# Optimization experiments

Measured on AMD Instinct MI355X. Metric: run time of the kernel, lower is better.

The kernel has to match this reference:

```python
import jax, jax.numpy as jnp
import numpy as np

VOCAB = 267735
CUTOFFS = [0, 20000, 40000, 200000, 267735]
D_EMBED = 1024
D_PROJ = 1024
DIV_VAL = 4
EMB_SCALE = float(D_PROJ) ** 0.5


def setup_inputs() -> dict:
    key = jax.random.key(0)
    ks = jax.random.split(key, 9)
    input_ids = jax.random.randint(ks[0], (8, 2048), 0, VOCAB, dtype=jnp.int64)
    inp = {"input_ids": input_ids}
    for i in range(4):
        l, r = CUTOFFS[i], CUTOFFS[i + 1]
        d_i = D_EMBED // (DIV_VAL ** i)
        inp[f"emb{i}"] = jax.random.normal(ks[1 + 2 * i], (r - l, d_i), dtype=jnp.float32) * 0.02
        inp[f"proj{i}"] = jax.random.normal(ks[2 + 2 * i], (D_PROJ, d_i), dtype=jnp.float32) * 0.02
    return inp


def reference(input_ids, emb0, emb1, emb2, emb3, proj0, proj1, proj2, proj3):
    tables = [emb0, emb1, emb2, emb3]
    projs = [proj0, proj1, proj2, proj3]
    out = jnp.zeros(input_ids.shape + (D_PROJ,), dtype=jnp.float32)
    for i in range(4):
        l, r = CUTOFFS[i], CUTOFFS[i + 1]
        mask = (input_ids >= l) & (input_ids < r)                     # [B,S]
        idx = jnp.clip(input_ids - l, 0, r - l - 1)                   # [B,S]
        emb_i = tables[i][idx]                                        # [B,S,d_i]
        proj_i = jnp.einsum('bse,de->bsd', emb_i, projs[i])           # [B,S,D]
        out = out + jnp.where(mask[..., None], proj_i, 0.0)
    return out * EMB_SCALE
```

## Files before the change

### kernel.cpp

```cpp
#include <hip/hip_runtime.h>


constexpr int NTOK  = 16384;
constexpr int DPROJ = 1024;
constexpr float EMB_SCALE = 32.0f;

typedef __attribute__((ext_vector_type(8))) short short8;
typedef __attribute__((ext_vector_type(4))) float float4v;

__global__ __launch_bounds__(256) void partition_kernel(
    const int* __restrict__ ids, int* __restrict__ cnt, int* __restrict__ lists)
{
    int t = blockIdx.x * 256 + threadIdx.x;
    int id = ids[t];
    int c = (id >= 200000) ? 3 : (id >= 40000) ? 2 : (id >= 20000) ? 1 : 0;
    int lane = threadIdx.x & 63;
    unsigned long long lt = (1ull << lane) - 1ull;
    int pos = 0;
#pragma unroll
    for (int i = 0; i < 4; ++i) {
        unsigned long long m = __ballot(c == i);
        int b = 0;
        if (lane == 0 && m) b = atomicAdd(&cnt[i], (int)__popcll(m));
        b = __shfl(b, 0);
        if (c == i) pos = b + (int)__popcll(m & lt);
    }
    lists[c * NTOK + pos] = t;
}

__device__ __forceinline__ short f2bf(float f) {
    unsigned u = __builtin_bit_cast(unsigned, f);
    u += 0x7FFFu + ((u >> 16) & 1u);
    return (short)(u >> 16);
}

template<int D>
__device__ __forceinline__ void gemm_tile(
    const int* __restrict__ ids,
    const float* __restrict__ emb,
    const float* __restrict__ proj,
    const int* __restrict__ list,
    int count, int lo,
    float* __restrict__ out,
    short (*Asm)[40], short (*Bsm)[40], int* smTok, int* smRow)
{
    const int m0 = blockIdx.y * 64;
    if (m0 >= count) return;
    const int n0 = blockIdx.x * 128;
    const int tid  = threadIdx.x;
    const int lane = tid & 63;
    const int wv   = tid >> 6;
    const int col  = lane & 15;
    const int quad = lane >> 4;

    if (tid < 64) {
        int m = m0 + tid;
        int tok = (m < count) ? list[m] : -1;
        smTok[tid] = tok;
        smRow[tid] = (tok >= 0) ? (ids[tok] - lo) : 0;
    }
    __syncthreads();

    const int ar = tid >> 2, ac = (tid & 3) * 8;
    const int br = tid >> 1, bc = (tid & 1) * 16;
    const float* arow = emb  + (size_t)smRow[ar] * D + ac;
    const float* brow = proj + (size_t)(n0 + br) * D + bc;

    float4v acc[4][2] = {};

    constexpr int CHUNKS = (D + 31) / 32;
    for (int kc = 0; kc < CHUNKS; ++kc) {
        const int k0 = kc * 32;
        float4 a0 = {}, a1 = {}, b0 = {}, b1 = {}, b2 = {}, b3 = {};
        if (ac + 0  < D || D >= 32) {  }
        if (D >= 32 || ac + 0  < D) a0 = *(const float4*)(arow + k0);
        if (D >= 32 || ac + 4  < D) a1 = *(const float4*)(arow + k0 + 4);
        if (D >= 32 || bc + 0  < D) b0 = *(const float4*)(brow + k0);
        if (D >= 32 || bc + 4  < D) b1 = *(const float4*)(brow + k0 + 4);
        if (D >= 32 || bc + 8  < D) b2 = *(const float4*)(brow + k0 + 8);
        if (D >= 32 || bc + 12 < D) b3 = *(const float4*)(brow + k0 + 12);
        if (D == 16) {
            if (ac >= 16) { a0 = float4{}; a1 = float4{}; }
            if (bc >= 16) { b0 = float4{}; b1 = float4{}; b2 = float4{}; b3 = float4{}; }
        }
        __syncthreads();
        {
            short8 va = { f2bf(a0.x), f2bf(a0.y), f2bf(a0.z), f2bf(a0.w),
                          f2bf(a1.x), f2bf(a1.y), f2bf(a1.z), f2bf(a1.w) };
            *(short8*)&Asm[ar][ac] = va;
            short8 vb0 = { f2bf(b0.x), f2bf(b0.y), f2bf(b0.z), f2bf(b0.w),
                           f2bf(b1.x), f2bf(b1.y), f2bf(b1.z), f2bf(b1.w) };
            short8 vb1 = { f2bf(b2.x), f2bf(b2.y), f2bf(b2.z), f2bf(b2.w),
                           f2bf(b3.x), f2bf(b3.y), f2bf(b3.z), f2bf(b3.w) };
            *(short8*)&Bsm[br][bc]     = vb0;
            *(short8*)&Bsm[br][bc + 8] = vb1;
        }
        __syncthreads();

        short8 af[4], bf[2];
#pragma unroll
        for (int m = 0; m < 4; ++m)
            af[m] = *(const short8*)&Asm[m * 16 + col][quad * 8];
#pragma unroll
        for (int n = 0; n < 2; ++n)
            bf[n] = *(const short8*)&Bsm[wv * 32 + n * 16 + col][quad * 8];
#pragma unroll
        for (int m = 0; m < 4; ++m)
#pragma unroll
            for (int n = 0; n < 2; ++n)
                acc[m][n] = __builtin_amdgcn_mfma_f32_16x16x32_bf16(
                    af[m], bf[n], acc[m][n], 0, 0, 0);
    }

#pragma unroll
    for (int m = 0; m < 4; ++m) {
#pragma unroll
        for (int r = 0; r < 4; ++r) {
            int tok = smTok[m * 16 + quad * 4 + r];
            if (tok < 0) continue;
            float* op = out + (size_t)tok * DPROJ + n0 + wv * 32 + col;
            op[0]  = acc[m][0][r] * EMB_SCALE;
            op[16] = acc[m][1][r] * EMB_SCALE;
        }
    }
}

__global__ __launch_bounds__(256) void adaptive_emb_gemm(
    const int* __restrict__ ids,
    const float* __restrict__ e0, const float* __restrict__ p0,
    const float* __restrict__ e1, const float* __restrict__ p1,
    const float* __restrict__ e2, const float* __restrict__ p2,
    const float* __restrict__ e3, const float* __restrict__ p3,
    const int* __restrict__ cnt, const int* __restrict__ lists,
    float* __restrict__ out)
{
    __shared__ short Asm[64][40];
    __shared__ short Bsm[128][40];
    __shared__ int smTok[64];
    __shared__ int smRow[64];

    switch (blockIdx.z) {
    case 0: gemm_tile<1024>(ids, e0, p0, lists,          cnt[0], 0,      out, Asm, Bsm, smTok, smRow); break;
    case 1: gemm_tile<256> (ids, e1, p1, lists + NTOK,   cnt[1], 20000,  out, Asm, Bsm, smTok, smRow); break;
    case 2: gemm_tile<64>  (ids, e2, p2, lists + 2*NTOK, cnt[2], 40000,  out, Asm, Bsm, smTok, smRow); break;
    case 3: gemm_tile<16>  (ids, e3, p3, lists + 3*NTOK, cnt[3], 200000, out, Asm, Bsm, smTok, smRow); break;
    }
}

extern "C" void kernel_launch(void* const* d_in, const int* in_sizes, int n_in,
                              void* d_out, int out_size, void* d_ws, size_t ws_size,
                              hipStream_t stream) {
    const int*   ids = (const int*)d_in[0];
    const float* e0  = (const float*)d_in[1];
    const float* p0  = (const float*)d_in[2];
    const float* e1  = (const float*)d_in[3];
    const float* p1  = (const float*)d_in[4];
    const float* e2  = (const float*)d_in[5];
    const float* p2  = (const float*)d_in[6];
    const float* e3  = (const float*)d_in[7];
    const float* p3  = (const float*)d_in[8];
    float* out = (float*)d_out;

    int* cnt   = (int*)d_ws;
    int* lists = cnt + 4;

    hipMemsetAsync(cnt, 0, 4 * sizeof(int), stream);
    partition_kernel<<<dim3(NTOK / 256), 256, 0, stream>>>(ids, cnt, lists);

    dim3 grid(DPROJ / 128, NTOK / 64, 4);
    adaptive_emb_gemm<<<grid, 256, 0, stream>>>(
        ids, e0, p0, e1, p1, e2, p2, e3, p3, cnt, lists, out);
}
```

Before: 229.5 us.

## Load MFMA fragments straight from global memory with register double-buffering

Drops the shared-memory staging of A and B tiles. Each lane now loads its own MFMA fragment rows directly from global memory and converts them to bf16 in registers, with a two-stage register double buffer that prefetches the next K chunk. This removes two barriers per chunk and the LDS traffic. The cost is redundant global loads across waves: each A row is read by all four waves and B is no longer cooperatively loaded. The grid axes are swapped so token tiles vary fastest, and launch bounds now request 3 blocks per CU.

```diff
diff --git a/kernel.cpp b/kernel.cpp
--- a/kernel.cpp
+++ b/kernel.cpp
@@ -34,6 +34,12 @@
     return (short)(u >> 16);
 }
 
+__device__ __forceinline__ short8 cvt8(float4 a, float4 b) {
+    short8 r = { f2bf(a.x), f2bf(a.y), f2bf(a.z), f2bf(a.w),
+                 f2bf(b.x), f2bf(b.y), f2bf(b.z), f2bf(b.w) };
+    return r;
+}
+
 template<int D>
 __device__ __forceinline__ void gemm_tile(
     const int* __restrict__ ids,
@@ -42,16 +48,17 @@
     const int* __restrict__ list,
     int count, int lo,
     float* __restrict__ out,
-    short (*Asm)[40], short (*Bsm)[40], int* smTok, int* smRow)
+    int* smTok, int* smRow)
 {
-    const int m0 = blockIdx.y * 64;
+    const int m0 = blockIdx.x * 64;
     if (m0 >= count) return;
-    const int n0 = blockIdx.x * 128;
+    const int n0 = blockIdx.y * 128;
     const int tid  = threadIdx.x;
     const int lane = tid & 63;
     const int wv   = tid >> 6;
     const int col  = lane & 15;
     const int quad = lane >> 4;
+    const int kq   = quad * 8;
 
     if (tid < 64) {
         int m = m0 + tid;
@@ -61,55 +68,66 @@
     }
     __syncthreads();
 
-    const int ar = tid >> 2, ac = (tid & 3) * 8;
-    const int br = tid >> 1, bc = (tid & 1) * 16;
-    const float* arow = emb  + (size_t)smRow[ar] * D + ac;
-    const float* brow = proj + (size_t)(n0 + br) * D + bc;
+    const float* aptr[4];
+#pragma unroll
+    for (int m = 0; m < 4; ++m)
+        aptr[m] = emb + (size_t)smRow[m * 16 + col] * D + kq;
+    const float* bptr[2];
+#pragma unroll
+    for (int n = 0; n < 2; ++n)
+        bptr[n] = proj + (size_t)(n0 + wv * 32 + n * 16 + col) * D + kq;
+
+    const bool kvalid = (D >= 32) || (kq < D);
 
     float4v acc[4][2] = {};
+    float4 A0[4][2], B0[2][2], A1[4][2], B1[2][2];
 
-    constexpr int CHUNKS = (D + 31) / 32;
-    for (int kc = 0; kc < CHUNKS; ++kc) {
-        const int k0 = kc * 32;
-        float4 a0 = {}, a1 = {}, b0 = {}, b1 = {}, b2 = {}, b3 = {};
-        if (ac + 0  < D || D >= 32) {  }
-        if (D >= 32 || ac + 0  < D) a0 = *(const float4*)(arow + k0);
-        if (D >= 32 || ac + 4  < D) a1 = *(const float4*)(arow + k0 + 4);
-        if (D >= 32 || bc + 0  < D) b0 = *(const float4*)(brow + k0);
-        if (D >= 32 || bc + 4  < D) b1 = *(const float4*)(brow + k0 + 4);
-        if (D >= 32 || bc + 8  < D) b2 = *(const float4*)(brow + k0 + 8);
-        if (D >= 32 || bc + 12 < D) b3 = *(const float4*)(brow + k0 + 12);
-        if (D == 16) {
-            if (ac >= 16) { a0 = float4{}; a1 = float4{}; }
-            if (bc >= 16) { b0 = float4{}; b1 = float4{}; b2 = float4{}; b3 = float4{}; }
+    auto loadc = [&](int kc, float4 (&A)[4][2], float4 (&B)[2][2]) {
+        const int off = kc * 32;
+#pragma unroll
+        for (int m = 0; m < 4; ++m) {
+            if (kvalid) {
+                A[m][0] = *(const float4*)(aptr[m] + off);
+                A[m][1] = *(const float4*)(aptr[m] + off + 4);
+            } else {
+                A[m][0] = float4{}; A[m][1] = float4{};
+            }
         }
-        __syncthreads();
-        {
-            short8 va = { f2bf(a0.x), f2bf(a0.y), f2bf(a0.z), f2bf(a0.w),
-                          f2bf(a1.x), f2bf(a1.y), f2bf(a1.z), f2bf(a1.w) };
-            *(short8*)&Asm[ar][ac] = va;
-            short8 vb0 = { f2bf(b0.x), f2bf(b0.y), f2bf(b0.z), f2bf(b0.w),
-                           f2bf(b1.x), f2bf(b1.y), f2bf(b1.z), f2bf(b1.w) };
-            short8 vb1 = { f2bf(b2.x), f2bf(b2.y), f2bf(b2.z), f2bf(b2.w),
-                           f2bf(b3.x), f2bf(b3.y), f2bf(b3.z), f2bf(b3.w) };
-            *(short8*)&Bsm[br][bc]     = vb0;
-            *(short8*)&Bsm[br][bc + 8] = vb1;
+#pragma unroll
+        for (int n = 0; n < 2; ++n) {
+            if (kvalid) {
+                B[n][0] = *(const float4*)(bptr[n] + off);
+                B[n][1] = *(const float4*)(bptr[n] + off + 4);
+            } else {
+                B[n][0] = float4{}; B[n][1] = float4{};
+            }
         }
-        __syncthreads();
+    };
 
+    auto computec = [&](float4 (&A)[4][2], float4 (&B)[2][2]) {
         short8 af[4], bf[2];
 #pragma unroll
-        for (int m = 0; m < 4; ++m)
-            af[m] = *(const short8*)&Asm[m * 16 + col][quad * 8];
+        for (int m = 0; m < 4; ++m) af[m] = cvt8(A[m][0], A[m][1]);
 #pragma unroll
-        for (int n = 0; n < 2; ++n)
-            bf[n] = *(const short8*)&Bsm[wv * 32 + n * 16 + col][quad * 8];
+        for (int n = 0; n < 2; ++n) bf[n] = cvt8(B[n][0], B[n][1]);
 #pragma unroll
         for (int m = 0; m < 4; ++m)
 #pragma unroll
             for (int n = 0; n < 2; ++n)
                 acc[m][n] = __builtin_amdgcn_mfma_f32_16x16x32_bf16(
                     af[m], bf[n], acc[m][n], 0, 0, 0);
+    };
+
+    constexpr int CHUNKS = (D + 31) / 32;
+    loadc(0, A0, B0);
+#pragma unroll 1
+    for (int kc = 0; kc < CHUNKS; kc += 2) {
+        if (kc + 1 < CHUNKS) loadc(kc + 1, A1, B1);
+        computec(A0, B0);
+        if (kc + 1 < CHUNKS) {
+            if (kc + 2 < CHUNKS) loadc(kc + 2, A0, B0);
+            computec(A1, B1);
+        }
     }
 
 #pragma unroll
@@ -125,7 +143,7 @@
     }
 }
 
-__global__ __launch_bounds__(256) void adaptive_emb_gemm(
+__global__ __launch_bounds__(256, 3) void adaptive_emb_gemm(
     const int* __restrict__ ids,
     const float* __restrict__ e0, const float* __restrict__ p0,
     const float* __restrict__ e1, const float* __restrict__ p1,
@@ -134,16 +152,14 @@
     const int* __restrict__ cnt, const int* __restrict__ lists,
     float* __restrict__ out)
 {
-    __shared__ short Asm[64][40];
-    __shared__ short Bsm[128][40];
     __shared__ int smTok[64];
     __shared__ int smRow[64];
 
     switch (blockIdx.z) {
-    case 0: gemm_tile<1024>(ids, e0, p0, lists,          cnt[0], 0,      out, Asm, Bsm, smTok, smRow); break;
-    case 1: gemm_tile<256> (ids, e1, p1, lists + NTOK,   cnt[1], 20000,  out, Asm, Bsm, smTok, smRow); break;
-    case 2: gemm_tile<64>  (ids, e2, p2, lists + 2*NTOK, cnt[2], 40000,  out, Asm, Bsm, smTok, smRow); break;
-    case 3: gemm_tile<16>  (ids, e3, p3, lists + 3*NTOK, cnt[3], 200000, out, Asm, Bsm, smTok, smRow); break;
+    case 0: gemm_tile<1024>(ids, e0, p0, lists,          cnt[0], 0,      out, smTok, smRow); break;
+    case 1: gemm_tile<256> (ids, e1, p1, lists + NTOK,   cnt[1], 20000,  out, smTok, smRow); break;
+    case 2: gemm_tile<64>  (ids, e2, p2, lists + 2*NTOK, cnt[2], 40000,  out, smTok, smRow); break;
+    case 3: gemm_tile<16>  (ids, e3, p3, lists + 3*NTOK, cnt[3], 200000, out, smTok, smRow); break;
     }
 }
 
@@ -167,7 +183,7 @@
     hipMemsetAsync(cnt, 0, 4 * sizeof(int), stream);
     partition_kernel<<<dim3(NTOK / 256), 256, 0, stream>>>(ids, cnt, lists);
 
-    dim3 grid(DPROJ / 128, NTOK / 64, 4);
+    dim3 grid(NTOK / 64, DPROJ / 128, 4);
     adaptive_emb_gemm<<<grid, 256, 0, stream>>>(
         ids, e0, p0, e1, p1, e2, p2, e3, p3, cnt, lists, out);
 }
```

Result: slower. 305.3 us (+33.1%).

## Double-buffer LDS tiles with two-deep register prefetch and swap grid axes

Applied to the files above, without the earlier changes.

Turns the K loop into a software pipeline. Global loads for chunk k+2 are issued into registers while the MFMAs for chunk k run, and chunk k+1 is written into the other LDS buffer, so each iteration needs one barrier instead of two. The grid axes are also swapped so that consecutive blocks walk along the token dimension instead of the projection columns, which changes launch order and cache locality and lets blocks with no tokens exit together. The cost is double the LDS per block and more registers for two staging sets, which may lower occupancy.

```diff
diff --git a/kernel.cpp b/kernel.cpp
--- a/kernel.cpp
+++ b/kernel.cpp
@@ -34,6 +34,14 @@
     return (short)(u >> 16);
 }
 
+__device__ __forceinline__ short8 cvt8(float4 a, float4 b) {
+    short8 r = { f2bf(a.x), f2bf(a.y), f2bf(a.z), f2bf(a.w),
+                 f2bf(b.x), f2bf(b.y), f2bf(b.z), f2bf(b.w) };
+    return r;
+}
+
+struct StageRegs { float4 a0, a1, b0, b1, b2, b3; };
+
 template<int D>
 __device__ __forceinline__ void gemm_tile(
     const int* __restrict__ ids,
@@ -42,11 +50,12 @@
     const int* __restrict__ list,
     int count, int lo,
     float* __restrict__ out,
-    short (*Asm)[40], short (*Bsm)[40], int* smTok, int* smRow)
+    short (&Asm)[2][64][40], short (&Bsm)[2][128][40],
+    int* smTok, int* smRow)
 {
-    const int m0 = blockIdx.y * 64;
+    const int m0 = blockIdx.x * 64;
     if (m0 >= count) return;
-    const int n0 = blockIdx.x * 128;
+    const int n0 = blockIdx.y * 128;
     const int tid  = threadIdx.x;
     const int lane = tid & 63;
     const int wv   = tid >> 6;
@@ -66,50 +75,60 @@
     const float* arow = emb  + (size_t)smRow[ar] * D + ac;
     const float* brow = proj + (size_t)(n0 + br) * D + bc;
 
+    auto stage = [&](int kc, StageRegs& R) {
+        const int k0 = kc * 32;
+        if (D >= 32 || ac + 8 <= D) {
+            R.a0 = *(const float4*)(arow + k0);
+            R.a1 = *(const float4*)(arow + k0 + 4);
+        } else { R.a0 = float4{}; R.a1 = float4{}; }
+        if (D >= 32 || bc + 16 <= D) {
+            R.b0 = *(const float4*)(brow + k0);
+            R.b1 = *(const float4*)(brow + k0 + 4);
+            R.b2 = *(const float4*)(brow + k0 + 8);
+            R.b3 = *(const float4*)(brow + k0 + 12);
+        } else { R.b0 = float4{}; R.b1 = float4{}; R.b2 = float4{}; R.b3 = float4{}; }
+    };
+
+    auto commit = [&](const StageRegs& R, int buf) {
+        *(short8*)&Asm[buf][ar][ac]     = cvt8(R.a0, R.a1);
+        *(short8*)&Bsm[buf][br][bc]     = cvt8(R.b0, R.b1);
+        *(short8*)&Bsm[buf][br][bc + 8] = cvt8(R.b2, R.b3);
+    };
+
     float4v acc[4][2] = {};
+    constexpr int CHUNKS = (D + 31) / 32;
 
-    constexpr int CHUNKS = (D + 31) / 32;
-    for (int kc = 0; kc < CHUNKS; ++kc) {
-        const int k0 = kc * 32;
-        float4 a0 = {}, a1 = {}, b0 = {}, b1 = {}, b2 = {}, b3 = {};
-        if (ac + 0  < D || D >= 32) {  }
-        if (D >= 32 || ac + 0  < D) a0 = *(const float4*)(arow + k0);
-        if (D >= 32 || ac + 4  < D) a1 = *(const float4*)(arow + k0 + 4);
-        if (D >= 32 || bc + 0  < D) b0 = *(const float4*)(brow + k0);
-        if (D >= 32 || bc + 4  < D) b1 = *(const float4*)(brow + k0 + 4);
-        if (D >= 32 || bc + 8  < D) b2 = *(const float4*)(brow + k0 + 8);
-        if (D >= 32 || bc + 12 < D) b3 = *(const float4*)(brow + k0 + 12);
-        if (D == 16) {
-            if (ac >= 16) { a0 = float4{}; a1 = float4{}; }
-            if (bc >= 16) { b0 = float4{}; b1 = float4{}; b2 = float4{}; b3 = float4{}; }
-        }
-        __syncthreads();
-        {
-            short8 va = { f2bf(a0.x), f2bf(a0.y), f2bf(a0.z), f2bf(a0.w),
-                          f2bf(a1.x), f2bf(a1.y), f2bf(a1.z), f2bf(a1.w) };
-            *(short8*)&Asm[ar][ac] = va;
-            short8 vb0 = { f2bf(b0.x), f2bf(b0.y), f2bf(b0.z), f2bf(b0.w),
-                           f2bf(b1.x), f2bf(b1.y), f2bf(b1.z), f2bf(b1.w) };
-            short8 vb1 = { f2bf(b2.x), f2bf(b2.y), f2bf(b2.z), f2bf(b2.w),
-                           f2bf(b3.x), f2bf(b3.y), f2bf(b3.z), f2bf(b3.w) };
-            *(short8*)&Bsm[br][bc]     = vb0;
-            *(short8*)&Bsm[br][bc + 8] = vb1;
-        }
-        __syncthreads();
+    StageRegs R0, R1;
+    stage(0, R0);
+    if (CHUNKS > 1) stage(1, R1);
+    commit(R0, 0);
+    asm volatile("s_waitcnt lgkmcnt(0)" ::: "memory");
+    __builtin_amdgcn_s_barrier();
 
+    auto body = [&](int kc, int buf, StageRegs& Rfree, StageRegs& Rnext) {
+        if (kc + 2 < CHUNKS) stage(kc + 2, Rfree);
         short8 af[4], bf[2];
 #pragma unroll
         for (int m = 0; m < 4; ++m)
-            af[m] = *(const short8*)&Asm[m * 16 + col][quad * 8];
+            af[m] = *(const short8*)&Asm[buf][m * 16 + col][quad * 8];
 #pragma unroll
         for (int n = 0; n < 2; ++n)
-            bf[n] = *(const short8*)&Bsm[wv * 32 + n * 16 + col][quad * 8];
+            bf[n] = *(const short8*)&Bsm[buf][wv * 32 + n * 16 + col][quad * 8];
 #pragma unroll
         for (int m = 0; m < 4; ++m)
 #pragma unroll
             for (int n = 0; n < 2; ++n)
                 acc[m][n] = __builtin_amdgcn_mfma_f32_16x16x32_bf16(
                     af[m], bf[n], acc[m][n], 0, 0, 0);
+        if (kc + 1 < CHUNKS) commit(Rnext, buf ^ 1);
+        asm volatile("s_waitcnt lgkmcnt(0)" ::: "memory");
+        __builtin_amdgcn_s_barrier();
+    };
+
+#pragma unroll 1
+    for (int kc = 0; kc < CHUNKS; kc += 2) {
+        body(kc, 0, R0, R1);
+        if (kc + 1 < CHUNKS) body(kc + 1, 1, R1, R0);
     }
 
 #pragma unroll
@@ -134,8 +153,8 @@
     const int* __restrict__ cnt, const int* __restrict__ lists,
     float* __restrict__ out)
 {
-    __shared__ short Asm[64][40];
-    __shared__ short Bsm[128][40];
+    __shared__ short Asm[2][64][40];
+    __shared__ short Bsm[2][128][40];
     __shared__ int smTok[64];
     __shared__ int smRow[64];
 
@@ -167,7 +186,7 @@
     hipMemsetAsync(cnt, 0, 4 * sizeof(int), stream);
     partition_kernel<<<dim3(NTOK / 256), 256, 0, stream>>>(ids, cnt, lists);
 
-    dim3 grid(DPROJ / 128, NTOK / 64, 4);
+    dim3 grid(NTOK / 64, DPROJ / 128, 4);
     adaptive_emb_gemm<<<grid, 256, 0, stream>>>(
         ids, e0, p0, e1, p1, e2, p2, e3, p3, cnt, lists, out);
 }
```

New measurement: 233.9 us. About the same (+1.9%).

## Split-K the largest embedding cluster across four z-slices with atomic accumulation

Applied to the files above, without the earlier changes.

Splits the K=1024 GEMM of cluster 0 into four slices of 256, launched as separate z-planes that accumulate into the output with float atomicAdd. The partition kernel now zeroes the output rows of cluster-0 tokens so the atomics start from zero. This removes the long serial K loop that made cluster-0 blocks the tail of the grid. In exchange it adds atomic traffic, a zeroing pass, and more launched blocks, many of which exit early. The atomic summation order is also nondeterministic.

```diff
diff --git a/kernel.cpp b/kernel.cpp
--- a/kernel.cpp
+++ b/kernel.cpp
@@ -9,7 +9,8 @@
 typedef __attribute__((ext_vector_type(4))) float float4v;
 
 __global__ __launch_bounds__(256) void partition_kernel(
-    const int* __restrict__ ids, int* __restrict__ cnt, int* __restrict__ lists)
+    const int* __restrict__ ids, int* __restrict__ cnt, int* __restrict__ lists,
+    float* __restrict__ out)
 {
     int t = blockIdx.x * 256 + threadIdx.x;
     int id = ids[t];
@@ -26,6 +27,16 @@
         if (c == i) pos = b + (int)__popcll(m & lt);
     }
     lists[c * NTOK + pos] = t;
+
+    unsigned long long mz = __ballot(c == 0);
+    int wbase = t & ~63;
+    while (mz) {
+        int src = __ffsll(mz) - 1; mz &= mz - 1;
+        float4* op = (float4*)(out + (size_t)(wbase + src) * DPROJ);
+        float4 z = {0.f, 0.f, 0.f, 0.f};
+#pragma unroll
+        for (int j = 0; j < 4; ++j) op[lane + 64 * j] = z;
+    }
 }
 
 __device__ __forceinline__ short f2bf(float f) {
@@ -34,13 +45,13 @@
     return (short)(u >> 16);
 }
 
-template<int D>
+template<int D, int NC, bool ATOMIC>
 __device__ __forceinline__ void gemm_tile(
     const int* __restrict__ ids,
     const float* __restrict__ emb,
     const float* __restrict__ proj,
     const int* __restrict__ list,
-    int count, int lo,
+    int count, int lo, int kbase,
     float* __restrict__ out,
     short (*Asm)[40], short (*Bsm)[40], int* smTok, int* smRow)
 {
@@ -68,11 +79,9 @@
 
     float4v acc[4][2] = {};
 
-    constexpr int CHUNKS = (D + 31) / 32;
-    for (int kc = 0; kc < CHUNKS; ++kc) {
-        const int k0 = kc * 32;
+    for (int kc = 0; kc < NC; ++kc) {
+        const int k0 = (kbase + kc) * 32;
         float4 a0 = {}, a1 = {}, b0 = {}, b1 = {}, b2 = {}, b3 = {};
-        if (ac + 0  < D || D >= 32) {  }
         if (D >= 32 || ac + 0  < D) a0 = *(const float4*)(arow + k0);
         if (D >= 32 || ac + 4  < D) a1 = *(const float4*)(arow + k0 + 4);
         if (D >= 32 || bc + 0  < D) b0 = *(const float4*)(brow + k0);
@@ -119,8 +128,13 @@
             int tok = smTok[m * 16 + quad * 4 + r];
             if (tok < 0) continue;
             float* op = out + (size_t)tok * DPROJ + n0 + wv * 32 + col;
-            op[0]  = acc[m][0][r] * EMB_SCALE;
-            op[16] = acc[m][1][r] * EMB_SCALE;
+            if constexpr (ATOMIC) {
+                atomicAdd(op,      acc[m][0][r] * EMB_SCALE);
+                atomicAdd(op + 16, acc[m][1][r] * EMB_SCALE);
+            } else {
+                op[0]  = acc[m][0][r] * EMB_SCALE;
+                op[16] = acc[m][1][r] * EMB_SCALE;
+            }
         }
     }
 }
@@ -139,11 +153,19 @@
     __shared__ int smTok[64];
     __shared__ int smRow[64];
 
-    switch (blockIdx.z) {
-    case 0: gemm_tile<1024>(ids, e0, p0, lists,          cnt[0], 0,      out, Asm, Bsm, smTok, smRow); break;
-    case 1: gemm_tile<256> (ids, e1, p1, lists + NTOK,   cnt[1], 20000,  out, Asm, Bsm, smTok, smRow); break;
-    case 2: gemm_tile<64>  (ids, e2, p2, lists + 2*NTOK, cnt[2], 40000,  out, Asm, Bsm, smTok, smRow); break;
-    case 3: gemm_tile<16>  (ids, e3, p3, lists + 3*NTOK, cnt[3], 200000, out, Asm, Bsm, smTok, smRow); break;
+    const int z = blockIdx.z;
+    if (z < 4) {
+        gemm_tile<1024, 8, true>(ids, e0, p0, lists, cnt[0], 0, z * 8,
+                                 out, Asm, Bsm, smTok, smRow);
+    } else if (z == 4) {
+        gemm_tile<256, 8, false>(ids, e1, p1, lists + NTOK, cnt[1], 20000, 0,
+                                 out, Asm, Bsm, smTok, smRow);
+    } else if (z == 5) {
+        gemm_tile<64, 2, false>(ids, e2, p2, lists + 2 * NTOK, cnt[2], 40000, 0,
+                                out, Asm, Bsm, smTok, smRow);
+    } else {
+        gemm_tile<16, 1, false>(ids, e3, p3, lists + 3 * NTOK, cnt[3], 200000, 0,
+                                out, Asm, Bsm, smTok, smRow);
     }
 }
 
@@ -164,10 +186,9 @@
     int* cnt   = (int*)d_ws;
     int* lists = cnt + 4;
 
-    hipMemsetAsync(cnt, 0, 4 * sizeof(int), stream);
-    partition_kernel<<<dim3(NTOK / 256), 256, 0, stream>>>(ids, cnt, lists);
+    (void)hipMemsetAsync(cnt, 0, 4 * sizeof(int), stream);
+    partition_kernel<<<dim3(NTOK / 256), 256, 0, stream>>>(ids, cnt, lists, out);
 
-    dim3 grid(DPROJ / 128, NTOK / 64, 4);
-    adaptive_emb_gemm<<<grid, 256, 0, stream>>>(
+    adaptive_emb_gemm<<<dim3(DPROJ / 128, NTOK / 64, 7), 256, 0, stream>>>(
         ids, e0, p0, e1, p1, e2, p2, e3, p3, cnt, lists, out);
 }
```

New measurement: 220.5 us. 1.04x faster.
